# Kernel optimization log

Measured on AMD Instinct MI355X. Metric: run time of the kernel, lower is better.

The kernel has to match this reference:

```python
import jax, jax.numpy as jnp
import numpy as np

N = 131072        # total packed tokens
D = 256           # input_dim
E = 512           # embed_dim
B = 16            # number of batches (len(cu_seqlens)-1)
NLAYERS = 64      # max distinct layer ids per batch


def setup_inputs() -> dict:
    key = jax.random.key(0)
    ks = jax.random.split(key, 8)
    feats = jax.random.normal(ks[0], (N, D), dtype=jnp.float32)
    cu_seqlens = jnp.arange(0, N + 1, N // B, dtype=jnp.int32)  # [B+1]
    layer_ids = jax.random.randint(ks[1], (N,), 0, NLAYERS, dtype=jnp.int32)
    # Linear params stored as [in, out] (y = x @ W + b), matching torch Linear math.
    Wa = jax.random.normal(ks[2], (D, 1), jnp.float32) * 0.05
    ba = jnp.zeros((1,), jnp.float32)
    W1 = jax.random.normal(ks[3], (3 * D, E), jnp.float32) * 0.02
    b1 = jnp.zeros((E,), jnp.float32)
    W2 = jax.random.normal(ks[4], (E, D), jnp.float32) * 0.02
    b2 = jnp.zeros((D,), jnp.float32)
    Wc = jax.random.normal(ks[5], (2 * D, D), jnp.float32) * 0.02
    bc = jnp.zeros((D,), jnp.float32)
    return dict(feats=feats, cu_seqlens=cu_seqlens, layer_ids=layer_ids,
                Wa=Wa, ba=ba, W1=W1, b1=b1, W2=W2, b2=b2, Wc=Wc, bc=bc)


def _forward(feats, cu_seqlens, layer_ids, Wa, ba, W1, b1, W2, b2, Wc, bc):
    n = feats.shape[0]
    nseg = B * NLAYERS
    # batch id of each token from the cumulative sequence lengths
    batch_ids = jnp.searchsorted(cu_seqlens, jnp.arange(n, dtype=jnp.int32), side='right') - 1
    # global (batch, layer) segment id -> vectorizes the per-batch scatter loop
    seg = batch_ids * NLAYERS + layer_ids

    counts = jax.ops.segment_sum(jnp.ones((n,), feats.dtype), seg, num_segments=nseg)  # [nseg]
    sums = jax.ops.segment_sum(feats, seg, num_segments=nseg)                           # [nseg, D]
    avg_pool = sums / jnp.maximum(counts, 1.0)[:, None]
    max_pool = jax.ops.segment_max(feats, seg, num_segments=nseg)
    max_pool = jnp.where(counts[:, None] > 0, max_pool, 0.0)  # empty segments -> 0 (never gathered)

    # attention softmax over all tokens of each batch (dim=0 within the batch slice)
    logits = (feats @ Wa + ba)[:, 0]                                    # [n]
    m = jax.ops.segment_max(logits, batch_ids, num_segments=B)          # [B]
    e = jnp.exp(logits - m[batch_ids])
    z = jax.ops.segment_sum(e, batch_ids, num_segments=B)               # [B]
    w = e / z[batch_ids]                                                # [n]
    attention_pool = jax.ops.segment_sum(feats * w[:, None], seg, num_segments=nseg)

    pooled = jnp.concatenate([avg_pool, max_pool, attention_pool], axis=1)  # [nseg, 3D]
    h = jax.nn.gelu(pooled @ W1 + b1, approximate=False)
    layer_feats = h @ W2 + b2                                               # [nseg, D]

    gathered = layer_feats[seg]                                             # [n, D]
    out = jnp.concatenate([gathered, feats], axis=1) @ Wc + bc              # [n, D]
    return out


def reference(feats, cu_seqlens, layer_ids, Wa, ba, W1, b1, W2, b2, Wc, bc):
    return _forward(feats, cu_seqlens, layer_ids, Wa, ba, W1, b1, W2, b2, Wc, bc)
```

## Files before the change

### kernel.cpp

```cpp
#include <hip/hip_runtime.h>
#include <hip/hip_bf16.h>
#include <math.h>

#define NTOK 131072
#define DIM  256
#define EDIM 512
#define NB   16
#define NL   64
#define NSEG (NB*NL)
#define K3D  768
#define K2D  512
#define HB   64
#define K4CH 256

typedef __attribute__((ext_vector_type(8))) short short8;
typedef __attribute__((ext_vector_type(4))) float f32x4;

static __device__ __forceinline__ unsigned fcode(float x){
  unsigned b = __float_as_uint(x);
  return (b & 0x80000000u) ? ~b : (b | 0x80000000u);
}
static __device__ __forceinline__ float fdecode(unsigned c){
  unsigned b = (c & 0x80000000u) ? (c ^ 0x80000000u) : ~c;
  return __uint_as_float(b);
}
#define NEG_INF_CODE 0x007FFFFFu

static __device__ __forceinline__ short f2bf(float x){
  union { __hip_bfloat16 h; short s; } u; u.h = __float2bfloat16(x); return u.s;
}
static __device__ __forceinline__ float bf2f(short s){
  union { float f; unsigned u; } u; u.u = ((unsigned)(unsigned short)s) << 16; return u.f;
}

__global__ __launch_bounds__(256) void k0_transpose(const float* __restrict__ W1, const float* __restrict__ W2,
                                                    const float* __restrict__ Wc,
                                                    short* __restrict__ W1t, short* __restrict__ W2t,
                                                    short* __restrict__ Wct, unsigned* __restrict__ bmax){
  if (blockIdx.x == 0 && threadIdx.x < NB) bmax[threadIdx.x] = NEG_INF_CODE;
  __shared__ short tile[64][65];
  int b = blockIdx.x;
  const float* src; short* dst; int K, N, kt, nt;
  if (b < 96){ src=W1; dst=W1t; K=768; N=512; kt=b/8;  nt=b%8;  }
  else if (b < 128){ int c=b-96;  src=W2; dst=W2t; K=512; N=256; kt=c/4; nt=c%4; }
  else             { int c=b-128; src=Wc; dst=Wct; K=512; N=256; kt=c/4; nt=c%4; }
  int k0 = kt*64, n0 = nt*64;
  for (int e = threadIdx.x; e < 4096; e += 256){
    int r = e >> 6, c = e & 63;
    tile[c][r] = f2bf(src[(size_t)(k0+r)*N + n0 + c]);
  }
  __syncthreads();
  for (int e = threadIdx.x; e < 4096; e += 256){
    int r = e >> 6, c = e & 63;
    dst[(size_t)(n0+r)*K + k0 + c] = tile[r][c];
  }
}

template<int WRITEB>
__global__ __launch_bounds__(256) void k1_logits(const float* __restrict__ feats, const int* __restrict__ cu,
    const int* __restrict__ layer_ids, const float* __restrict__ Wa, const float* __restrict__ ba,
    float* __restrict__ logits, int* __restrict__ seg, unsigned* __restrict__ bmax,
    short* __restrict__ featsb){
  __shared__ int      lcu[NB];
  __shared__ unsigned lbm[NB];
  int tid = threadIdx.x;
  if (tid < NB){ lcu[tid] = cu[tid+1]; lbm[tid] = NEG_INF_CODE; }
  int s = tid & 15;
  int rowoff = tid >> 4;
  float4 w0 = *(const float4*)(Wa + s*4);
  float4 w1 = *(const float4*)(Wa + 64 + s*4);
  float4 w2 = *(const float4*)(Wa + 128 + s*4);
  float4 w3 = *(const float4*)(Wa + 192 + s*4);
  float bav = ba[0];
  __syncthreads();
#pragma unroll
  for (int it = 0; it < 4; ++it){
    int r = (blockIdx.x + it*2048)*16 + rowoff;
    const float4* fp = (const float4*)(feats + (size_t)r*DIM);
    float4 x0 = fp[s], x1 = fp[16+s], x2 = fp[32+s], x3 = fp[48+s];
    float a = x0.x*w0.x + x0.y*w0.y + x0.z*w0.z + x0.w*w0.w
            + x1.x*w1.x + x1.y*w1.y + x1.z*w1.z + x1.w*w1.w
            + x2.x*w2.x + x2.y*w2.y + x2.z*w2.z + x2.w*w2.w
            + x3.x*w3.x + x3.y*w3.y + x3.z*w3.z + x3.w*w3.w;
    if (WRITEB){
      short4* ob = (short4*)(featsb + (size_t)r*DIM);
      short4 v;
      v.x=f2bf(x0.x); v.y=f2bf(x0.y); v.z=f2bf(x0.z); v.w=f2bf(x0.w); ob[s]    = v;
      v.x=f2bf(x1.x); v.y=f2bf(x1.y); v.z=f2bf(x1.z); v.w=f2bf(x1.w); ob[16+s] = v;
      v.x=f2bf(x2.x); v.y=f2bf(x2.y); v.z=f2bf(x2.z); v.w=f2bf(x2.w); ob[32+s] = v;
      v.x=f2bf(x3.x); v.y=f2bf(x3.y); v.z=f2bf(x3.z); v.w=f2bf(x3.w); ob[48+s] = v;
    }
    a += __shfl_xor(a, 1);
    a += __shfl_xor(a, 2);
    a += __shfl_xor(a, 4);
    a += __shfl_xor(a, 8);
    if (s == 0){
      float lg = a + bav;
      logits[r] = lg;
      int b = 0;
#pragma unroll
      for (int j = 0; j < NB-1; ++j) b += (lcu[j] <= r) ? 1 : 0;
      seg[r] = b*NL + layer_ids[r];
      atomicMax(&lbm[b], fcode(lg));
    }
  }
  __syncthreads();
  if (tid < NB && lbm[tid] != NEG_INF_CODE) atomicMax(&bmax[tid], lbm[tid]);
}

__global__ __launch_bounds__(256) void k23_hist_z(const int* __restrict__ seg, int* __restrict__ hist,
    const float* __restrict__ logits, const int* __restrict__ cu,
    const unsigned* __restrict__ bmax, float* __restrict__ bz){
  __shared__ int h[NSEG];
  int bid = blockIdx.x;
  if (bid < HB){
    for (int i = threadIdx.x; i < NSEG; i += 256) h[i] = 0;
    __syncthreads();
    int base = bid * (NTOK/HB);
    for (int i = threadIdx.x; i < NTOK/HB; i += 256) atomicAdd(&h[seg[base+i]], 1);
    __syncthreads();
    for (int i = threadIdx.x; i < NSEG; i += 256) hist[(size_t)bid*NSEG + i] = h[i];
  } else {
    float* red = (float*)h;
    int b = bid - HB;
    int s = cu[b], e = cu[b+1];
    float m = fdecode(bmax[b]);
    float acc = 0.f;
    for (int i = s + threadIdx.x; i < e; i += 256)
      acc += expf(logits[i] - m);
    red[threadIdx.x] = acc; __syncthreads();
    for (int off = 128; off; off >>= 1){
      if (threadIdx.x < off) red[threadIdx.x] += red[threadIdx.x + off];
      __syncthreads();
    }
    if (threadIdx.x == 0) bz[b] = red[0];
  }
}

__global__ __launch_bounds__(1024) void k3b_scan(int* __restrict__ hist, int* __restrict__ segstart){
  __shared__ int sc[NSEG];
  int s = threadIdx.x;
  int tot = 0;
#pragma unroll
  for (int b = 0; b < HB; ++b) tot += hist[(size_t)b*NSEG + s];
  sc[s] = tot; __syncthreads();
  for (int off = 1; off < NSEG; off <<= 1){
    int v = (s >= off) ? sc[s-off] : 0;
    __syncthreads();
    sc[s] += v;
    __syncthreads();
  }
  int segbase = sc[s] - tot;
  segstart[s] = segbase;
  if (s == 0) segstart[NSEG] = NTOK;
  int run = segbase;
#pragma unroll
  for (int b = 0; b < HB; ++b){
    int c = hist[(size_t)b*NSEG + s];
    hist[(size_t)b*NSEG + s] = run;
    run += c;
  }
}

__global__ __launch_bounds__(256) void k3c_scatter(const int* __restrict__ seg, const int* __restrict__ hist,
                                                   int* __restrict__ sorted){
  __shared__ int cur[NSEG];
  for (int i = threadIdx.x; i < NSEG; i += 256) cur[i] = hist[(size_t)blockIdx.x*NSEG + i];
  __syncthreads();
  int base = blockIdx.x * (NTOK/HB);
  for (int i = threadIdx.x; i < NTOK/HB; i += 256){
    int sg = seg[base+i];
    int p = atomicAdd(&cur[sg], 1);
    sorted[p] = base+i;
  }
}

template<int USEB>
__global__ __launch_bounds__(256) void k4_pool(const float* __restrict__ feats, const short* __restrict__ featsb,
    const int* __restrict__ sorted, const int* __restrict__ segstart,
    const float* __restrict__ logits, const unsigned* __restrict__ bmax, const float* __restrict__ bz,
    short* __restrict__ pooledb){
  __shared__ float redS[4][DIM];
  __shared__ float redM[4][DIM];
  __shared__ float redA[4][DIM];
  __shared__ int   ltok[K4CH];
  __shared__ float lwgt[K4CH];
  int sgi = blockIdx.x;
  int b = sgi >> 6;
  int s = segstart[sgi], e = segstart[sgi+1];
  int cnt = e - s;
  float m = fdecode(bmax[b]);
  float invz = 1.0f / bz[b];
  int lane = threadIdx.x & 63, grp = threadIdx.x >> 6;
  float4 sum = make_float4(0.f,0.f,0.f,0.f), att = make_float4(0.f,0.f,0.f,0.f);
  float4 mx  = make_float4(-INFINITY,-INFINITY,-INFINITY,-INFINITY);
  for (int c0 = s; c0 < e; c0 += K4CH){
    int csz = min(K4CH, e - c0);
    for (int j = threadIdx.x; j < csz; j += 256){
      int t = sorted[c0 + j];
      ltok[j] = t;
      lwgt[j] = expf(logits[t] - m) * invz;
    }
    __syncthreads();
    for (int j = grp; j < csz; j += 4){
      int tok = ltok[j];
      float w = lwgt[j];
      float4 x;
      if (USEB){
        short4 h = *(const short4*)(featsb + (size_t)tok*DIM + lane*4);
        x = make_float4(bf2f(h.x), bf2f(h.y), bf2f(h.z), bf2f(h.w));
      } else {
        x = *(const float4*)(feats + (size_t)tok*DIM + lane*4);
      }
      sum.x += x.x; sum.y += x.y; sum.z += x.z; sum.w += x.w;
      mx.x = fmaxf(mx.x, x.x); mx.y = fmaxf(mx.y, x.y);
      mx.z = fmaxf(mx.z, x.z); mx.w = fmaxf(mx.w, x.w);
      att.x += x.x*w; att.y += x.y*w; att.z += x.z*w; att.w += x.w*w;
    }
    __syncthreads();
  }
  *(float4*)&redS[grp][lane*4] = sum;
  *(float4*)&redM[grp][lane*4] = mx;
  *(float4*)&redA[grp][lane*4] = att;
  __syncthreads();
  int d = threadIdx.x;
  float rs = redS[0][d] + redS[1][d] + redS[2][d] + redS[3][d];
  float rm = fmaxf(fmaxf(redM[0][d], redM[1][d]), fmaxf(redM[2][d], redM[3][d]));
  float ra = redA[0][d] + redA[1][d] + redA[2][d] + redA[3][d];
  float inv = 1.0f / (float)(cnt > 1 ? cnt : 1);
  size_t rb_ = (size_t)sgi * K3D;
  pooledb[rb_ + d]         = f2bf(rs * inv);
  pooledb[rb_ + DIM + d]   = f2bf(cnt > 0 ? rm : 0.f);
  pooledb[rb_ + 2*DIM + d] = f2bf(ra);
}

template<int GELU>
__global__ __launch_bounds__(256) void gemm64(const short* __restrict__ A, const short* __restrict__ Bt,
    const float* __restrict__ bias, short* __restrict__ Cout, int K, int ldc){
  __shared__ short lA[64][40];
  __shared__ short lB[64][40];
  int tid = threadIdx.x;
  int wave = tid >> 6, lane = tid & 63;
  int wm = wave >> 1, wn = wave & 1;
  int rb = blockIdx.x * 64, cb = blockIdx.y * 64;
  int l15 = lane & 15, lg = lane >> 4;
  f32x4 acc[2][2] = {};
  int srow = tid >> 2, skg = tid & 3;
  for (int ks = 0; ks < K; ks += 32){
    __syncthreads();
    *(short8*)&lA[srow][skg*8] = *(const short8*)(A  + (size_t)(rb+srow)*K + ks + skg*8);
    *(short8*)&lB[srow][skg*8] = *(const short8*)(Bt + (size_t)(cb+srow)*K + ks + skg*8);
    __syncthreads();
    short8 af[2], bf[2];
#pragma unroll
    for (int f = 0; f < 2; ++f){
      af[f] = *(const short8*)&lA[wm*32 + f*16 + l15][lg*8];
      bf[f] = *(const short8*)&lB[wn*32 + f*16 + l15][lg*8];
    }
#pragma unroll
    for (int fm = 0; fm < 2; ++fm)
#pragma unroll
      for (int fn = 0; fn < 2; ++fn)
        acc[fm][fn] = __builtin_amdgcn_mfma_f32_16x16x32_bf16(af[fm], bf[fn], acc[fm][fn], 0, 0, 0);
  }
#pragma unroll
  for (int fm = 0; fm < 2; ++fm)
#pragma unroll
    for (int fn = 0; fn < 2; ++fn){
      int col = cb + wn*32 + fn*16 + l15;
      float bcv = bias[col];
#pragma unroll
      for (int r = 0; r < 4; ++r){
        int row = rb + wm*32 + fm*16 + lg*4 + r;
        float v = acc[fm][fn][r] + bcv;
        if (GELU) v = 0.5f * v * (1.0f + erff(v * 0.70710678118f));
        Cout[(size_t)row*ldc + col] = f2bf(v);
      }
    }
}

template<int USEB>
__global__ __launch_bounds__(512, 4) void k5_final(const float* __restrict__ feats,
    const short* __restrict__ featsb, const short* __restrict__ lfb,
    const int* __restrict__ seg, const short* __restrict__ Wct, const float* __restrict__ bc,
    float* __restrict__ out){
  __shared__ short lA[2][128][72];
  __shared__ short lB[2][128][72];
  int tid = threadIdx.x;
  int wave = tid >> 6, lane = tid & 63;
  int wm = wave >> 2, wn = wave & 3;
  int bid = (int)blockIdx.x;
  int swz = (bid & 7) * 256 + (bid >> 3);
  int rb = (swz >> 1) * 128;
  int cb = (swz & 1) * 128;
  int l15 = lane & 15, lg = lane >> 4;
  int arow0 = tid >> 3, arow1 = (tid >> 3) + 64, akg = tid & 7;
  const short* lfbp0 = lfb + (size_t)seg[rb + arow0]*DIM + akg*8;
  const short* lfbp1 = lfb + (size_t)seg[rb + arow1]*DIM + akg*8;
  const short* fbp0  = featsb + (size_t)(rb + arow0)*DIM + akg*8;
  const short* fbp1  = featsb + (size_t)(rb + arow1)*DIM + akg*8;
  const float* ffp0  = feats  + (size_t)(rb + arow0)*DIM + akg*8;
  const float* ffp1  = feats  + (size_t)(rb + arow1)*DIM + akg*8;
  const short* wp0 = Wct + (size_t)(cb + arow0)*K2D + akg*8;
  const short* wp1 = Wct + (size_t)(cb + arow1)*K2D + akg*8;
  short8 ra0, ra1, rb0, rb1; float4 fa00, fa01, fa10, fa11;
  auto LOAD = [&](int t){
    if (t < 4){
      ra0 = *(const short8*)(lfbp0 + t*64);
      ra1 = *(const short8*)(lfbp1 + t*64);
    } else if (USEB){
      ra0 = *(const short8*)(fbp0 + (t-4)*64);
      ra1 = *(const short8*)(fbp1 + (t-4)*64);
    } else {
      const float* p0 = ffp0 + (size_t)(t-4)*64; fa00 = *(const float4*)p0; fa01 = *(const float4*)(p0+4);
      const float* p1 = ffp1 + (size_t)(t-4)*64; fa10 = *(const float4*)p1; fa11 = *(const float4*)(p1+4);
    }
    rb0 = *(const short8*)(wp0 + t*64);
    rb1 = *(const short8*)(wp1 + t*64);
  };
  auto WRITE = [&](int t){
    int buf = t & 1;
    if (!USEB && t >= 4){
      short8 v;
      v[0]=f2bf(fa00.x); v[1]=f2bf(fa00.y); v[2]=f2bf(fa00.z); v[3]=f2bf(fa00.w);
      v[4]=f2bf(fa01.x); v[5]=f2bf(fa01.y); v[6]=f2bf(fa01.z); v[7]=f2bf(fa01.w);
      *(short8*)&lA[buf][arow0][akg*8] = v;
      v[0]=f2bf(fa10.x); v[1]=f2bf(fa10.y); v[2]=f2bf(fa10.z); v[3]=f2bf(fa10.w);
      v[4]=f2bf(fa11.x); v[5]=f2bf(fa11.y); v[6]=f2bf(fa11.z); v[7]=f2bf(fa11.w);
      *(short8*)&lA[buf][arow1][akg*8] = v;
    } else {
      *(short8*)&lA[buf][arow0][akg*8] = ra0;
      *(short8*)&lA[buf][arow1][akg*8] = ra1;
    }
    *(short8*)&lB[buf][arow0][akg*8] = rb0;
    *(short8*)&lB[buf][arow1][akg*8] = rb1;
  };
  f32x4 acc[4][2] = {};
  LOAD(0); WRITE(0); LOAD(1);
  __syncthreads();
  for (int ks = 0; ks < 8; ++ks){
    int cur = ks & 1;
    if (ks < 7) WRITE(ks+1);
    if (ks < 6) LOAD(ks+2);
#pragma unroll
    for (int kk = 0; kk < 2; ++kk){
      short8 af[4], bf[2];
#pragma unroll
      for (int f = 0; f < 4; ++f)
        af[f] = *(const short8*)&lA[cur][wm*64 + f*16 + l15][kk*32 + lg*8];
#pragma unroll
      for (int f = 0; f < 2; ++f)
        bf[f] = *(const short8*)&lB[cur][wn*32 + f*16 + l15][kk*32 + lg*8];
#pragma unroll
      for (int fm = 0; fm < 4; ++fm)
#pragma unroll
        for (int fn = 0; fn < 2; ++fn)
          acc[fm][fn] = __builtin_amdgcn_mfma_f32_16x16x32_bf16(af[fm], bf[fn], acc[fm][fn], 0, 0, 0);
    }
    __syncthreads();
  }
#pragma unroll
  for (int fm = 0; fm < 4; ++fm)
#pragma unroll
    for (int fn = 0; fn < 2; ++fn){
      int col = cb + wn*32 + fn*16 + l15;
      float bcv = bc[col];
#pragma unroll
      for (int r = 0; r < 4; ++r){
        int row = rb + wm*64 + fm*16 + lg*4 + r;
        out[(size_t)row*DIM + col] = acc[fm][fn][r] + bcv;
      }
    }
}

extern "C" void kernel_launch(void* const* d_in, const int* in_sizes, int n_in,
                              void* d_out, int out_size, void* d_ws, size_t ws_size,
                              hipStream_t stream){
  const float* feats     = (const float*)d_in[0];
  const int*   cu        = (const int*)d_in[1];
  const int*   layer_ids = (const int*)d_in[2];
  const float* Wa        = (const float*)d_in[3];
  const float* ba        = (const float*)d_in[4];
  const float* W1        = (const float*)d_in[5];
  const float* b1        = (const float*)d_in[6];
  const float* W2        = (const float*)d_in[7];
  const float* b2        = (const float*)d_in[8];
  const float* Wc        = (const float*)d_in[9];
  const float* bc        = (const float*)d_in[10];
  float* out = (float*)d_out;

  char* w = (char*)d_ws;
  auto alloc = [&](size_t bytes)->char*{ char* p = w; w += (bytes + 255) & ~255ull; return p; };
  float*    logits  = (float*)   alloc((size_t)NTOK*4);
  int*      seg     = (int*)     alloc((size_t)NTOK*4);
  int*      sorted  = (int*)     alloc((size_t)NTOK*4);
  int*      hist    = (int*)     alloc((size_t)NSEG*HB*4);
  int*      segstart= (int*)     alloc((size_t)(NSEG+1)*4);
  unsigned* bmax    = (unsigned*)alloc(NB*4);
  float*    bz      = (float*)   alloc(NB*4);
  short*    W1t     = (short*)   alloc((size_t)512*768*2);
  short*    W2t     = (short*)   alloc((size_t)256*512*2);
  short*    Wct     = (short*)   alloc((size_t)256*512*2);
  short*    pooledb = (short*)   alloc((size_t)NSEG*K3D*2);
  short*    hb      = (short*)   alloc((size_t)NSEG*EDIM*2);
  short*    lfb     = (short*)   alloc((size_t)NSEG*DIM*2);
  short*    featsb  = (short*)   alloc((size_t)NTOK*DIM*2);
  size_t need = (size_t)(w - (char*)d_ws);
  bool useb = (ws_size >= need);

  k0_transpose<<<dim3(160), dim3(256), 0, stream>>>(W1, W2, Wc, W1t, W2t, Wct, bmax);
  if (useb)
    k1_logits<1><<<dim3(2048), dim3(256), 0, stream>>>(feats, cu, layer_ids, Wa, ba, logits, seg, bmax, featsb);
  else
    k1_logits<0><<<dim3(2048), dim3(256), 0, stream>>>(feats, cu, layer_ids, Wa, ba, logits, seg, bmax, featsb);
  k23_hist_z<<<dim3(HB + NB), dim3(256), 0, stream>>>(seg, hist, logits, cu, bmax, bz);
  k3b_scan<<<dim3(1), dim3(1024), 0, stream>>>(hist, segstart);
  k3c_scatter<<<dim3(HB), dim3(256), 0, stream>>>(seg, hist, sorted);
  if (useb)
    k4_pool<1><<<dim3(NSEG), dim3(256), 0, stream>>>(feats, featsb, sorted, segstart, logits, bmax, bz, pooledb);
  else
    k4_pool<0><<<dim3(NSEG), dim3(256), 0, stream>>>(feats, featsb, sorted, segstart, logits, bmax, bz, pooledb);
  gemm64<1><<<dim3(16, 8), dim3(256), 0, stream>>>(pooledb, W1t, b1, hb, 768, 512);
  gemm64<0><<<dim3(16, 4), dim3(256), 0, stream>>>(hb, W2t, b2, lfb, 512, 256);
  if (useb)
    k5_final<1><<<dim3(2048), dim3(512), 0, stream>>>(feats, featsb, lfb, seg, Wct, bc, out);
  else
    k5_final<0><<<dim3(2048), dim3(512), 0, stream>>>(feats, featsb, lfb, seg, Wct, bc, out);
}
```

Before: 178.1 us.

## Precompute per-segment Wc projection and replace histogram matrix with atomic counts

The final GEMM's gathered half (layer_feats[seg] @ Wc_top + bc) is precomputed once per segment (1024×256) in a new small MFMA kernel and added in the epilogue via a seg-indexed fp32 lookup. This halves the K dimension of the big per-token GEMM (512→256). The per-block histogram matrix is also replaced with global atomic segment counts and a per-block atomic reservation in scatter. That removes the 64-way hist read/write loops in the scan, at the cost of a non-deterministic token order within segments and an extra histogram pass in scatter.

After: 157.1 us. -11.8%, faster.

```diff
diff --git a/kernel.cpp b/kernel.cpp
--- a/kernel.cpp
+++ b/kernel.cpp
@@ -36,8 +36,12 @@
 __global__ __launch_bounds__(256) void k0_transpose(const float* __restrict__ W1, const float* __restrict__ W2,
                                                     const float* __restrict__ Wc,
                                                     short* __restrict__ W1t, short* __restrict__ W2t,
-                                                    short* __restrict__ Wct, unsigned* __restrict__ bmax){
-  if (blockIdx.x == 0 && threadIdx.x < NB) bmax[threadIdx.x] = NEG_INF_CODE;
+                                                    short* __restrict__ Wct, unsigned* __restrict__ bmax,
+                                                    int* __restrict__ segcnt){
+  if (blockIdx.x == 0){
+    if (threadIdx.x < NB) bmax[threadIdx.x] = NEG_INF_CODE;
+    for (int i = threadIdx.x; i < NSEG; i += 256) segcnt[i] = 0;
+  }
   __shared__ short tile[64][65];
   int b = blockIdx.x;
   const float* src; short* dst; int K, N, kt, nt;
@@ -108,7 +112,7 @@
   if (tid < NB && lbm[tid] != NEG_INF_CODE) atomicMax(&bmax[tid], lbm[tid]);
 }
 
-__global__ __launch_bounds__(256) void k23_hist_z(const int* __restrict__ seg, int* __restrict__ hist,
+__global__ __launch_bounds__(256) void k23_hist_z(const int* __restrict__ seg, int* __restrict__ segcnt,
     const float* __restrict__ logits, const int* __restrict__ cu,
     const unsigned* __restrict__ bmax, float* __restrict__ bz){
   __shared__ int h[NSEG];
@@ -119,7 +123,7 @@
     int base = bid * (NTOK/HB);
     for (int i = threadIdx.x; i < NTOK/HB; i += 256) atomicAdd(&h[seg[base+i]], 1);
     __syncthreads();
-    for (int i = threadIdx.x; i < NSEG; i += 256) hist[(size_t)bid*NSEG + i] = h[i];
+    for (int i = threadIdx.x; i < NSEG; i += 256){ int c = h[i]; if (c) atomicAdd(&segcnt[i], c); }
   } else {
     float* red = (float*)h;
     int b = bid - HB;
@@ -137,12 +141,11 @@
   }
 }
 
-__global__ __launch_bounds__(1024) void k3b_scan(int* __restrict__ hist, int* __restrict__ segstart){
+__global__ __launch_bounds__(1024) void k3b_scan(const int* __restrict__ segcnt, int* __restrict__ segstart,
+                                                 int* __restrict__ cur){
   __shared__ int sc[NSEG];
   int s = threadIdx.x;
-  int tot = 0;
-#pragma unroll
-  for (int b = 0; b < HB; ++b) tot += hist[(size_t)b*NSEG + s];
+  int tot = segcnt[s];
   sc[s] = tot; __syncthreads();
   for (int off = 1; off < NSEG; off <<= 1){
     int v = (s >= off) ? sc[s-off] : 0;
@@ -150,27 +153,28 @@
     sc[s] += v;
     __syncthreads();
   }
-  int segbase = sc[s] - tot;
-  segstart[s] = segbase;
+  int base = sc[s] - tot;
+  segstart[s] = base;
+  cur[s] = base;
   if (s == 0) segstart[NSEG] = NTOK;
-  int run = segbase;
-#pragma unroll
-  for (int b = 0; b < HB; ++b){
-    int c = hist[(size_t)b*NSEG + s];
-    hist[(size_t)b*NSEG + s] = run;
-    run += c;
-  }
-}
-
-__global__ __launch_bounds__(256) void k3c_scatter(const int* __restrict__ seg, const int* __restrict__ hist,
+}
+
+__global__ __launch_bounds__(256) void k3c_scatter(const int* __restrict__ seg, int* __restrict__ cur,
                                                    int* __restrict__ sorted){
-  __shared__ int cur[NSEG];
-  for (int i = threadIdx.x; i < NSEG; i += 256) cur[i] = hist[(size_t)blockIdx.x*NSEG + i];
+  __shared__ int h[NSEG];
+  for (int i = threadIdx.x; i < NSEG; i += 256) h[i] = 0;
   __syncthreads();
   int base = blockIdx.x * (NTOK/HB);
+  for (int i = threadIdx.x; i < NTOK/HB; i += 256) atomicAdd(&h[seg[base+i]], 1);
+  __syncthreads();
+  for (int i = threadIdx.x; i < NSEG; i += 256){
+    int c = h[i];
+    if (c) h[i] = atomicAdd(&cur[i], c);
+  }
+  __syncthreads();
   for (int i = threadIdx.x; i < NTOK/HB; i += 256){
     int sg = seg[base+i];
-    int p = atomicAdd(&cur[sg], 1);
+    int p = atomicAdd(&h[sg], 1);
     sorted[p] = base+i;
   }
 }
@@ -279,10 +283,52 @@
     }
 }
 
+__global__ __launch_bounds__(256) void k_lfp(const short* __restrict__ A, const short* __restrict__ Bt,
+    const float* __restrict__ bias, float* __restrict__ Cout){
+  __shared__ short lA[64][40];
+  __shared__ short lB[64][40];
+  int tid = threadIdx.x;
+  int wave = tid >> 6, lane = tid & 63;
+  int wm = wave >> 1, wn = wave & 1;
+  int rb = blockIdx.x * 64, cb = blockIdx.y * 64;
+  int l15 = lane & 15, lg = lane >> 4;
+  f32x4 acc[2][2] = {};
+  int srow = tid >> 2, skg = tid & 3;
+  for (int ks = 0; ks < 256; ks += 32){
+    __syncthreads();
+    *(short8*)&lA[srow][skg*8] = *(const short8*)(A  + (size_t)(rb+srow)*DIM + ks + skg*8);
+    *(short8*)&lB[srow][skg*8] = *(const short8*)(Bt + (size_t)(cb+srow)*K2D + ks + skg*8);
+    __syncthreads();
+    short8 af[2], bf[2];
+#pragma unroll
+    for (int f = 0; f < 2; ++f){
+      af[f] = *(const short8*)&lA[wm*32 + f*16 + l15][lg*8];
+      bf[f] = *(const short8*)&lB[wn*32 + f*16 + l15][lg*8];
+    }
+#pragma unroll
+    for (int fm = 0; fm < 2; ++fm)
+#pragma unroll
+      for (int fn = 0; fn < 2; ++fn)
+        acc[fm][fn] = __builtin_amdgcn_mfma_f32_16x16x32_bf16(af[fm], bf[fn], acc[fm][fn], 0, 0, 0);
+  }
+#pragma unroll
+  for (int fm = 0; fm < 2; ++fm)
+#pragma unroll
+    for (int fn = 0; fn < 2; ++fn){
+      int col = cb + wn*32 + fn*16 + l15;
+      float bcv = bias[col];
+#pragma unroll
+      for (int r = 0; r < 4; ++r){
+        int row = rb + wm*32 + fm*16 + lg*4 + r;
+        Cout[(size_t)row*DIM + col] = acc[fm][fn][r] + bcv;
+      }
+    }
+}
+
 template<int USEB>
 __global__ __launch_bounds__(512, 4) void k5_final(const float* __restrict__ feats,
-    const short* __restrict__ featsb, const short* __restrict__ lfb,
-    const int* __restrict__ seg, const short* __restrict__ Wct, const float* __restrict__ bc,
+    const short* __restrict__ featsb, const float* __restrict__ lfp,
+    const int* __restrict__ seg, const short* __restrict__ Wct,
     float* __restrict__ out){
   __shared__ short lA[2][128][72];
   __shared__ short lB[2][128][72];
@@ -295,32 +341,27 @@
   int cb = (swz & 1) * 128;
   int l15 = lane & 15, lg = lane >> 4;
   int arow0 = tid >> 3, arow1 = (tid >> 3) + 64, akg = tid & 7;
-  const short* lfbp0 = lfb + (size_t)seg[rb + arow0]*DIM + akg*8;
-  const short* lfbp1 = lfb + (size_t)seg[rb + arow1]*DIM + akg*8;
   const short* fbp0  = featsb + (size_t)(rb + arow0)*DIM + akg*8;
   const short* fbp1  = featsb + (size_t)(rb + arow1)*DIM + akg*8;
   const float* ffp0  = feats  + (size_t)(rb + arow0)*DIM + akg*8;
   const float* ffp1  = feats  + (size_t)(rb + arow1)*DIM + akg*8;
-  const short* wp0 = Wct + (size_t)(cb + arow0)*K2D + akg*8;
-  const short* wp1 = Wct + (size_t)(cb + arow1)*K2D + akg*8;
+  const short* wp0 = Wct + (size_t)(cb + arow0)*K2D + 256 + akg*8;
+  const short* wp1 = Wct + (size_t)(cb + arow1)*K2D + 256 + akg*8;
   short8 ra0, ra1, rb0, rb1; float4 fa00, fa01, fa10, fa11;
   auto LOAD = [&](int t){
-    if (t < 4){
-      ra0 = *(const short8*)(lfbp0 + t*64);
-      ra1 = *(const short8*)(lfbp1 + t*64);
-    } else if (USEB){
-      ra0 = *(const short8*)(fbp0 + (t-4)*64);
-      ra1 = *(const short8*)(fbp1 + (t-4)*64);
+    if (USEB){
+      ra0 = *(const short8*)(fbp0 + t*64);
+      ra1 = *(const short8*)(fbp1 + t*64);
     } else {
-      const float* p0 = ffp0 + (size_t)(t-4)*64; fa00 = *(const float4*)p0; fa01 = *(const float4*)(p0+4);
-      const float* p1 = ffp1 + (size_t)(t-4)*64; fa10 = *(const float4*)p1; fa11 = *(const float4*)(p1+4);
+      const float* p0 = ffp0 + (size_t)t*64; fa00 = *(const float4*)p0; fa01 = *(const float4*)(p0+4);
+      const float* p1 = ffp1 + (size_t)t*64; fa10 = *(const float4*)p1; fa11 = *(const float4*)(p1+4);
     }
     rb0 = *(const short8*)(wp0 + t*64);
     rb1 = *(const short8*)(wp1 + t*64);
   };
   auto WRITE = [&](int t){
     int buf = t & 1;
-    if (!USEB && t >= 4){
+    if (!USEB){
       short8 v;
       v[0]=f2bf(fa00.x); v[1]=f2bf(fa00.y); v[2]=f2bf(fa00.z); v[3]=f2bf(fa00.w);
       v[4]=f2bf(fa01.x); v[5]=f2bf(fa01.y); v[6]=f2bf(fa01.z); v[7]=f2bf(fa01.w);
@@ -338,10 +379,10 @@
   f32x4 acc[4][2] = {};
   LOAD(0); WRITE(0); LOAD(1);
   __syncthreads();
-  for (int ks = 0; ks < 8; ++ks){
+  for (int ks = 0; ks < 4; ++ks){
     int cur = ks & 1;
-    if (ks < 7) WRITE(ks+1);
-    if (ks < 6) LOAD(ks+2);
+    if (ks < 3) WRITE(ks+1);
+    if (ks < 2) LOAD(ks+2);
 #pragma unroll
     for (int kk = 0; kk < 2; ++kk){
       short8 af[4], bf[2];
@@ -360,17 +401,19 @@
     __syncthreads();
   }
 #pragma unroll
-  for (int fm = 0; fm < 4; ++fm)
+  for (int fm = 0; fm < 4; ++fm){
+    int rbase = rb + wm*64 + fm*16 + lg*4;
+    int4 sg4 = *(const int4*)(seg + rbase);
+    int sgs[4] = {sg4.x, sg4.y, sg4.z, sg4.w};
 #pragma unroll
     for (int fn = 0; fn < 2; ++fn){
       int col = cb + wn*32 + fn*16 + l15;
-      float bcv = bc[col];
 #pragma unroll
       for (int r = 0; r < 4; ++r){
-        int row = rb + wm*64 + fm*16 + lg*4 + r;
-        out[(size_t)row*DIM + col] = acc[fm][fn][r] + bcv;
+        out[(size_t)(rbase+r)*DIM + col] = acc[fm][fn][r] + lfp[(size_t)sgs[r]*DIM + col];
       }
     }
+  }
 }
 
 extern "C" void kernel_launch(void* const* d_in, const int* in_sizes, int n_in,
@@ -394,8 +437,9 @@
   float*    logits  = (float*)   alloc((size_t)NTOK*4);
   int*      seg     = (int*)     alloc((size_t)NTOK*4);
   int*      sorted  = (int*)     alloc((size_t)NTOK*4);
-  int*      hist    = (int*)     alloc((size_t)NSEG*HB*4);
+  int*      segcnt  = (int*)     alloc((size_t)NSEG*4);
   int*      segstart= (int*)     alloc((size_t)(NSEG+1)*4);
+  int*      cur     = (int*)     alloc((size_t)NSEG*4);
   unsigned* bmax    = (unsigned*)alloc(NB*4);
   float*    bz      = (float*)   alloc(NB*4);
   short*    W1t     = (short*)   alloc((size_t)512*768*2);
@@ -404,26 +448,28 @@
   short*    pooledb = (short*)   alloc((size_t)NSEG*K3D*2);
   short*    hb      = (short*)   alloc((size_t)NSEG*EDIM*2);
   short*    lfb     = (short*)   alloc((size_t)NSEG*DIM*2);
+  float*    lfp     = (float*)   alloc((size_t)NSEG*DIM*4);
   short*    featsb  = (short*)   alloc((size_t)NTOK*DIM*2);
   size_t need = (size_t)(w - (char*)d_ws);
   bool useb = (ws_size >= need);
 
-  k0_transpose<<<dim3(160), dim3(256), 0, stream>>>(W1, W2, Wc, W1t, W2t, Wct, bmax);
+  k0_transpose<<<dim3(160), dim3(256), 0, stream>>>(W1, W2, Wc, W1t, W2t, Wct, bmax, segcnt);
   if (useb)
     k1_logits<1><<<dim3(2048), dim3(256), 0, stream>>>(feats, cu, layer_ids, Wa, ba, logits, seg, bmax, featsb);
   else
     k1_logits<0><<<dim3(2048), dim3(256), 0, stream>>>(feats, cu, layer_ids, Wa, ba, logits, seg, bmax, featsb);
-  k23_hist_z<<<dim3(HB + NB), dim3(256), 0, stream>>>(seg, hist, logits, cu, bmax, bz);
-  k3b_scan<<<dim3(1), dim3(1024), 0, stream>>>(hist, segstart);
-  k3c_scatter<<<dim3(HB), dim3(256), 0, stream>>>(seg, hist, sorted);
+  k23_hist_z<<<dim3(HB + NB), dim3(256), 0, stream>>>(seg, segcnt, logits, cu, bmax, bz);
+  k3b_scan<<<dim3(1), dim3(1024), 0, stream>>>(segcnt, segstart, cur);
+  k3c_scatter<<<dim3(HB), dim3(256), 0, stream>>>(seg, cur, sorted);
   if (useb)
     k4_pool<1><<<dim3(NSEG), dim3(256), 0, stream>>>(feats, featsb, sorted, segstart, logits, bmax, bz, pooledb);
   else
     k4_pool<0><<<dim3(NSEG), dim3(256), 0, stream>>>(feats, featsb, sorted, segstart, logits, bmax, bz, pooledb);
   gemm64<1><<<dim3(16, 8), dim3(256), 0, stream>>>(pooledb, W1t, b1, hb, 768, 512);
   gemm64<0><<<dim3(16, 4), dim3(256), 0, stream>>>(hb, W2t, b2, lfb, 512, 256);
+  k_lfp<<<dim3(16, 4), dim3(256), 0, stream>>>(lfb, Wct, bc, lfp);
   if (useb)
-    k5_final<1><<<dim3(2048), dim3(512), 0, stream>>>(feats, featsb, lfb, seg, Wct, bc, out);
+    k5_final<1><<<dim3(2048), dim3(512), 0, stream>>>(feats, featsb, lfp, seg, Wct, out);
   else
-    k5_final<0><<<dim3(2048), dim3(512), 0, stream>>>(feats, featsb, lfb, seg, Wct, bc, out);
-}
+    k5_final<0><<<dim3(2048), dim3(512), 0, stream>>>(feats, featsb, lfp, seg, Wct, out);
+}
```
